# Optimization experiments

Hardware: AMD Instinct MI355X
Metric: run time of the kernel (lower is better)

## Reference

```python
import jax, jax.numpy as jnp
import numpy as np

CE_W, DICE_W, BD_W = 1.0, 3.0, 2.0   # combined-loss lambdas
BPW = 10.0                            # boundary pixel weight
SMOOTH = 1e-6                         # dice smoothing
# cv2.getStructuringElement(cv2.MORPH_ELLIPSE, (5,5))
ELLIPSE5 = np.array([[0,0,1,0,0],
                     [1,1,1,1,1],
                     [1,1,1,1,1],
                     [1,1,1,1,1],
                     [0,0,1,0,0]], dtype=bool)


def setup_inputs() -> dict:
    key = jax.random.key(0)
    k1, k2 = jax.random.split(key)
    B, C, H, W = 8, 8, 512, 1024
    pred = jax.random.normal(k1, (B, C, H, W), dtype=jnp.float32)
    target = jax.random.randint(k2, (B, H, W), 0, C).astype(jnp.int32)
    return {"pred": pred, "target": target}


def _morph(mask, is_dilate):
    """Grayscale dilate/erode with 5x5 ellipse SE (matches cv2 default border:
    padding value never wins the max/min)."""
    pad_val = 0 if is_dilate else jnp.iinfo(jnp.int32).max
    p = jnp.pad(mask, ((0, 0), (2, 2), (2, 2)), constant_values=pad_val)
    H, W = mask.shape[1], mask.shape[2]
    out = None
    for dy in range(5):
        for dx in range(5):
            if not ELLIPSE5[dy, dx]:
                continue
            s = p[:, dy:dy + H, dx:dx + W]
            if out is None:
                out = s
            else:
                out = jnp.maximum(out, s) if is_dilate else jnp.minimum(out, s)
    return out


def reference(pred, target):
    B, C, H, W = pred.shape
    logp = jax.nn.log_softmax(pred, axis=1)                         # (B,C,H,W)
    # per-pixel cross entropy
    ce_map = -jnp.take_along_axis(logp, target[:, None], axis=1)[:, 0]  # (B,H,W)
    ce = ce_map.mean()
    # dice over softmax probs vs one-hot target
    probs = jnp.exp(logp)
    onehot = jax.nn.one_hot(target, C, dtype=pred.dtype, axis=1)    # (B,C,H,W)
    inter = jnp.sum(probs * onehot, axis=(2, 3))                    # (B,C)
    card = jnp.sum(probs, axis=(2, 3)) + jnp.sum(onehot, axis=(2, 3))
    dice = 1.0 - jnp.mean((2.0 * inter + SMOOTH) / (card + SMOOTH))
    # boundary mask = morphological gradient of the label map
    t = target.astype(jnp.int32)
    boundary = _morph(t, True) - _morph(t, False)                   # (B,H,W)
    wmap = jnp.where(boundary > 0, jnp.float32(BPW), jnp.float32(1.0))
    bd = jnp.mean(ce_map * wmap)
    return CE_W * ce + DICE_W * dice + BD_W * bd
```

## Files before the change

### kernel.cpp

```cpp
#include <hip/hip_runtime.h>
#include <math.h>

constexpr int B = 8, C = 8, H = 512, W = 1024;
constexpr int RH = 2;
constexpr int NT = 256;
constexpr float BPW = 10.0f;
constexpr float SMOOTH = 1e-6f;

constexpr int ACC_N = 2 + 3 * B * C;

__device__ __forceinline__ unsigned win_or5(unsigned lo, unsigned mid, unsigned hi) {
    unsigned long long a = ((unsigned long long)mid << 32) | lo;
    unsigned long long b = ((unsigned long long)hi << 32) | mid;
    return (unsigned)(a >> 16) | (unsigned)(a >> 24) | mid |
           (unsigned)(b >> 8) | (unsigned)(b >> 16);
}

__device__ __forceinline__ unsigned pack_row(const int* __restrict__ tb, int gh, int gc) {
    if (gh < 0 || gh >= H || gc < 0 || gc >= W) return 0u;
    const int4 t4 = *reinterpret_cast<const int4*>(tb + (size_t)gh * W + gc);
    return (1u << t4.x) | ((1u << t4.y) << 8) | ((1u << t4.z) << 16) | ((1u << t4.w) << 24);
}

__global__ __launch_bounds__(NT)
void loss_main(const float* __restrict__ pred, const int* __restrict__ target,
               float* __restrict__ acc) {
    __shared__ float sred[4][26];

    const int tid = threadIdx.x;
    const int h0 = blockIdx.x * RH;
    const int b  = blockIdx.y;
    const int gc = tid * 4;

    const int* tb = target + (size_t)b * H * W;
    const size_t plane = (size_t)H * W;
    const float* pb = pred + (size_t)b * C * plane + (size_t)h0 * W + gc;

    const unsigned c0 = pack_row(tb, h0 - 2, gc);
    const unsigned c1 = pack_row(tb, h0 - 1, gc);
    const unsigned c2 = pack_row(tb, h0,     gc);
    const unsigned c3 = pack_row(tb, h0 + 1, gc);
    const unsigned c4 = pack_row(tb, h0 + 2, gc);
    const unsigned c5 = pack_row(tb, h0 + 3, gc);
    const unsigned l0 = pack_row(tb, h0 - 1, gc - 4);
    const unsigned l1 = pack_row(tb, h0,     gc - 4);
    const unsigned l2 = pack_row(tb, h0 + 1, gc - 4);
    const unsigned l3 = pack_row(tb, h0 + 2, gc - 4);
    const unsigned r0 = pack_row(tb, h0 - 1, gc + 4);
    const unsigned r1 = pack_row(tb, h0,     gc + 4);
    const unsigned r2 = pack_row(tb, h0 + 1, gc + 4);
    const unsigned r3 = pack_row(tb, h0 + 2, gc + 4);

    float4 xa[C], xb[C];
#pragma unroll
    for (int c = 0; c < C; ++c) xa[c] = *reinterpret_cast<const float4*>(pb + c * plane);
#pragma unroll
    for (int c = 0; c < C; ++c) xb[c] = *reinterpret_cast<const float4*>(pb + c * plane + W);

    float ce_s = 0.f, bd_s = 0.f;
    float p_s[C], in_s[C];
    unsigned cnt = 0u;
#pragma unroll
    for (int c = 0; c < C; ++c) { p_s[c] = 0.f; in_s[c] = 0.f; }

    const unsigned bmA = win_or5(l0 | l1 | l2, c1 | c2 | c3, r0 | r1 | r2) | c0 | c4;
    const unsigned bmB = win_or5(l1 | l2 | l3, c2 | c3 | c4, r1 | r2 | r3) | c1 | c5;

#pragma unroll
    for (int s = 0; s < 2; ++s) {
        const float4* x = (s == 0) ? xa : xb;
        const unsigned cmid = (s == 0) ? c2 : c3;
        const unsigned bm4  = (s == 0) ? bmA : bmB;

#pragma unroll
        for (int j = 0; j < 4; ++j) {
            const float x0 = (j==0)?x[0].x:(j==1)?x[0].y:(j==2)?x[0].z:x[0].w;
            const float x1 = (j==0)?x[1].x:(j==1)?x[1].y:(j==2)?x[1].z:x[1].w;
            const float x2 = (j==0)?x[2].x:(j==1)?x[2].y:(j==2)?x[2].z:x[2].w;
            const float x3 = (j==0)?x[3].x:(j==1)?x[3].y:(j==2)?x[3].z:x[3].w;
            const float x4 = (j==0)?x[4].x:(j==1)?x[4].y:(j==2)?x[4].z:x[4].w;
            const float x5 = (j==0)?x[5].x:(j==1)?x[5].y:(j==2)?x[5].z:x[5].w;
            const float x6 = (j==0)?x[6].x:(j==1)?x[6].y:(j==2)?x[6].z:x[6].w;
            const float x7 = (j==0)?x[7].x:(j==1)?x[7].y:(j==2)?x[7].z:x[7].w;

            const float e0 = __expf(x0), e1 = __expf(x1), e2 = __expf(x2), e3 = __expf(x3);
            const float e4 = __expf(x4), e5 = __expf(x5), e6 = __expf(x6), e7 = __expf(x7);
            const float sum = ((e0 + e1) + (e2 + e3)) + ((e4 + e5) + (e6 + e7));
            const float invs = __builtin_amdgcn_rcpf(sum);

            const unsigned cm  = (cmid >> (8 * j)) & 0xFFu;
            const unsigned bmj = (bm4  >> (8 * j)) & 0xFFu;
            const int t = 31 - __clz(cm);

            const float p0 = e0 * invs, p1 = e1 * invs, p2 = e2 * invs, p3 = e3 * invs;
            const float p4 = e4 * invs, p5 = e5 * invs, p6 = e6 * invs, p7 = e7 * invs;
            p_s[0] += p0; p_s[1] += p1; p_s[2] += p2; p_s[3] += p3;
            p_s[4] += p4; p_s[5] += p5; p_s[6] += p6; p_s[7] += p7;

            const bool b0 = (t == 0), b1 = (t == 1), b2 = (t == 2), b3 = (t == 3);
            const bool b4 = (t == 4), b5 = (t == 5), b6 = (t == 6), b7 = (t == 7);
            in_s[0] += b0 ? p0 : 0.f;  in_s[1] += b1 ? p1 : 0.f;
            in_s[2] += b2 ? p2 : 0.f;  in_s[3] += b3 ? p3 : 0.f;
            in_s[4] += b4 ? p4 : 0.f;  in_s[5] += b5 ? p5 : 0.f;
            in_s[6] += b6 ? p6 : 0.f;  in_s[7] += b7 ? p7 : 0.f;

            float pt = p0;
            pt = b1 ? p1 : pt;  pt = b2 ? p2 : pt;  pt = b3 ? p3 : pt;
            pt = b4 ? p4 : pt;  pt = b5 ? p5 : pt;  pt = b6 ? p6 : pt;
            pt = b7 ? p7 : pt;
            const float l = __logf(pt);
            const float wgt = (bmj & (bmj - 1u)) ? BPW : 1.f;
            ce_s -= l;
            bd_s = fmaf(-l, wgt, bd_s);
            cnt += 1u << (t << 2);
        }
    }

    float vals[26];
    vals[0] = ce_s; vals[1] = bd_s;
#pragma unroll
    for (int c = 0; c < C; ++c) {
        vals[2 + c]  = p_s[c];
        vals[10 + c] = in_s[c];
        vals[18 + c] = (float)((cnt >> (4 * c)) & 0xFu);
    }
#pragma unroll
    for (int k = 0; k < 26; ++k) {
        float v = vals[k];
#pragma unroll
        for (int off = 32; off > 0; off >>= 1) v += __shfl_down(v, off, 64);
        vals[k] = v;
    }
    const int lane = tid & 63, wid = tid >> 6;
    if (lane == 0) {
#pragma unroll
        for (int k = 0; k < 26; ++k) sred[wid][k] = vals[k];
    }
    __syncthreads();
    if (tid < 26) {
        const float v = sred[0][tid] + sred[1][tid] + sred[2][tid] + sred[3][tid];
        int gi;
        if (tid == 0)       gi = 0;
        else if (tid == 1)  gi = 1;
        else if (tid < 10)  gi = 2 + b * C + (tid - 2);
        else if (tid < 18)  gi = 2 + B * C + b * C + (tid - 10);
        else                gi = 2 + 2 * B * C + b * C + (tid - 18);
        atomicAdd(&acc[gi], v);
    }
}

__global__ void loss_final(const float* __restrict__ acc, float* __restrict__ out) {
    const int i = threadIdx.x;
    const float psum  = acc[2 + i];
    const float inter = acc[2 + B * C + i];
    const float cnt   = acc[2 + 2 * B * C + i];
    float d = (2.f * inter + SMOOTH) / (psum + cnt + SMOOTH);
#pragma unroll
    for (int off = 32; off > 0; off >>= 1) d += __shfl_down(d, off, 64);
    if (i == 0) {
        const float N = (float)B * H * W;
        const float ce = acc[0] / N;
        const float bd = acc[1] / N;
        const float dice = 1.f - d / (float)(B * C);
        out[0] = 1.0f * ce + 3.0f * dice + 2.0f * bd;
    }
}

extern "C" void kernel_launch(void* const* d_in, const int* in_sizes, int n_in,
                              void* d_out, int out_size, void* d_ws, size_t ws_size,
                              hipStream_t stream) {
    const float* pred = (const float*)d_in[0];
    const int* target = (const int*)d_in[1];
    float* acc = (float*)d_ws;
    float* out = (float*)d_out;

    hipMemsetAsync(acc, 0, ACC_N * sizeof(float), stream);

    dim3 grid(H / RH, B);
    loss_main<<<grid, NT, 0, stream>>>(pred, target, acc);
    loss_final<<<1, 64, 0, stream>>>(acc, out);
}
```

Before: 211.5 us.

## Stage packed label halo in LDS, process four rows per block, swizzle blocks

Each block now handles four rows instead of two. It packs the eight-row label halo into shared memory as one-hot bytes, so the left and right neighbour windows are read from LDS rather than through redundant global loads. Block indices are swizzled so that neighbouring launches fall in different images, and launch bounds request four blocks per SM. The cross-lane reduction is reshaped to finish with partial shuffles plus a strided LDS pass, which cuts the number of shuffle steps. The costs are an extra __syncthreads, more LDS use, and fewer blocks in flight.

```diff
diff --git a/kernel.cpp b/kernel.cpp
--- a/kernel.cpp
+++ b/kernel.cpp
@@ -2,12 +2,17 @@
 #include <math.h>
 
 constexpr int B = 8, C = 8, H = 512, W = 1024;
-constexpr int RH = 2;
+constexpr int RH = 4;
 constexpr int NT = 256;
 constexpr float BPW = 10.0f;
 constexpr float SMOOTH = 1e-6f;
 
 constexpr int ACC_N = 2 + 3 * B * C;
+
+constexpr int TROWS = RH + 4;
+constexpr int TSTRIDE = W + 8;
+constexpr int NVALS = 26;
+constexpr int PSTRIDE = 28;
 
 __device__ __forceinline__ unsigned win_or5(unsigned lo, unsigned mid, unsigned hi) {
     unsigned long long a = ((unsigned long long)mid << 32) | lo;
@@ -16,61 +21,68 @@
            (unsigned)(b >> 8) | (unsigned)(b >> 16);
 }
 
-__device__ __forceinline__ unsigned pack_row(const int* __restrict__ tb, int gh, int gc) {
-    if (gh < 0 || gh >= H || gc < 0 || gc >= W) return 0u;
-    const int4 t4 = *reinterpret_cast<const int4*>(tb + (size_t)gh * W + gc);
-    return (1u << t4.x) | ((1u << t4.y) << 8) | ((1u << t4.z) << 16) | ((1u << t4.w) << 24);
-}
-
-__global__ __launch_bounds__(NT)
+__global__ __launch_bounds__(NT, 4)
 void loss_main(const float* __restrict__ pred, const int* __restrict__ target,
                float* __restrict__ acc) {
-    __shared__ float sred[4][26];
+    __shared__ unsigned char tgt[TROWS * TSTRIDE];
+    __shared__ float sred[32 * PSTRIDE];
 
     const int tid = threadIdx.x;
-    const int h0 = blockIdx.x * RH;
-    const int b  = blockIdx.y;
+    const int lin = blockIdx.x + blockIdx.y * gridDim.x;
+    const int swz = (lin & 7) * 128 + (lin >> 3);
+    const int h0 = (swz & 127) * RH;
+    const int b  = swz >> 7;
     const int gc = tid * 4;
 
     const int* tb = target + (size_t)b * H * W;
     const size_t plane = (size_t)H * W;
-    const float* pb = pred + (size_t)b * C * plane + (size_t)h0 * W + gc;
-
-    const unsigned c0 = pack_row(tb, h0 - 2, gc);
-    const unsigned c1 = pack_row(tb, h0 - 1, gc);
-    const unsigned c2 = pack_row(tb, h0,     gc);
-    const unsigned c3 = pack_row(tb, h0 + 1, gc);
-    const unsigned c4 = pack_row(tb, h0 + 2, gc);
-    const unsigned c5 = pack_row(tb, h0 + 3, gc);
-    const unsigned l0 = pack_row(tb, h0 - 1, gc - 4);
-    const unsigned l1 = pack_row(tb, h0,     gc - 4);
-    const unsigned l2 = pack_row(tb, h0 + 1, gc - 4);
-    const unsigned l3 = pack_row(tb, h0 + 2, gc - 4);
-    const unsigned r0 = pack_row(tb, h0 - 1, gc + 4);
-    const unsigned r1 = pack_row(tb, h0,     gc + 4);
-    const unsigned r2 = pack_row(tb, h0 + 1, gc + 4);
-    const unsigned r3 = pack_row(tb, h0 + 2, gc + 4);
-
-    float4 xa[C], xb[C];
-#pragma unroll
-    for (int c = 0; c < C; ++c) xa[c] = *reinterpret_cast<const float4*>(pb + c * plane);
-#pragma unroll
-    for (int c = 0; c < C; ++c) xb[c] = *reinterpret_cast<const float4*>(pb + c * plane + W);
+
+    if (tid < 2 * TROWS) {
+        const int r = tid >> 1;
+        *reinterpret_cast<unsigned*>(&tgt[r * TSTRIDE + ((tid & 1) ? (4 + W) : 0)]) = 0u;
+    }
+#pragma unroll
+    for (int r = 0; r < TROWS; ++r) {
+        const int gh = h0 - 2 + r;
+        unsigned m = 0u;
+        if (gh >= 0 && gh < H) {
+            const int4 t4 = *reinterpret_cast<const int4*>(tb + (size_t)gh * W + gc);
+            m = (1u << t4.x) | ((1u << t4.y) << 8) | ((1u << t4.z) << 16) | ((1u << t4.w) << 24);
+        }
+        *reinterpret_cast<unsigned*>(&tgt[r * TSTRIDE + 4 + gc]) = m;
+    }
+    __syncthreads();
+
+    unsigned M[TROWS], L[TROWS], R[TROWS];
+#pragma unroll
+    for (int r = 0; r < TROWS; ++r)
+        M[r] = *reinterpret_cast<const unsigned*>(&tgt[r * TSTRIDE + 4 + gc]);
+#pragma unroll
+    for (int r = 1; r < TROWS - 1; ++r) {
+        L[r] = *reinterpret_cast<const unsigned*>(&tgt[r * TSTRIDE + gc]);
+        R[r] = *reinterpret_cast<const unsigned*>(&tgt[r * TSTRIDE + 8 + gc]);
+    }
 
     float ce_s = 0.f, bd_s = 0.f;
     float p_s[C], in_s[C];
-    unsigned cnt = 0u;
+    unsigned long long cnt = 0ull;
 #pragma unroll
     for (int c = 0; c < C; ++c) { p_s[c] = 0.f; in_s[c] = 0.f; }
 
-    const unsigned bmA = win_or5(l0 | l1 | l2, c1 | c2 | c3, r0 | r1 | r2) | c0 | c4;
-    const unsigned bmB = win_or5(l1 | l2 | l3, c2 | c3 | c4, r1 | r2 | r3) | c1 | c5;
-
-#pragma unroll
-    for (int s = 0; s < 2; ++s) {
-        const float4* x = (s == 0) ? xa : xb;
-        const unsigned cmid = (s == 0) ? c2 : c3;
-        const unsigned bm4  = (s == 0) ? bmA : bmB;
+    const float* pbase = pred + (size_t)b * C * plane + (size_t)h0 * W + gc;
+
+#pragma unroll
+    for (int s = 0; s < RH; ++s) {
+        float4 x[C];
+#pragma unroll
+        for (int c = 0; c < C; ++c)
+            x[c] = *reinterpret_cast<const float4*>(pbase + (size_t)c * plane + (size_t)s * W);
+
+        const unsigned Lor = L[s + 1] | L[s + 2] | L[s + 3];
+        const unsigned Mor = M[s + 1] | M[s + 2] | M[s + 3];
+        const unsigned Ror = R[s + 1] | R[s + 2] | R[s + 3];
+        const unsigned bm4  = win_or5(Lor, Mor, Ror) | M[s] | M[s + 4];
+        const unsigned cmid = M[s + 2];
 
 #pragma unroll
         for (int j = 0; j < 4; ++j) {
@@ -112,40 +124,50 @@
             const float wgt = (bmj & (bmj - 1u)) ? BPW : 1.f;
             ce_s -= l;
             bd_s = fmaf(-l, wgt, bd_s);
-            cnt += 1u << (t << 2);
+            cnt += 1ull << (t << 3);
         }
     }
 
-    float vals[26];
+    float vals[NVALS];
     vals[0] = ce_s; vals[1] = bd_s;
 #pragma unroll
     for (int c = 0; c < C; ++c) {
         vals[2 + c]  = p_s[c];
         vals[10 + c] = in_s[c];
-        vals[18 + c] = (float)((cnt >> (4 * c)) & 0xFu);
-    }
-#pragma unroll
-    for (int k = 0; k < 26; ++k) {
+        vals[18 + c] = (float)((unsigned)((cnt >> (8 * c)) & 0xFFull));
+    }
+#pragma unroll
+    for (int k = 0; k < NVALS; ++k) {
         float v = vals[k];
-#pragma unroll
-        for (int off = 32; off > 0; off >>= 1) v += __shfl_down(v, off, 64);
+        v += __shfl_down(v, 32, 64);
+        v += __shfl_down(v, 16, 64);
+        v += __shfl_down(v, 8, 64);
         vals[k] = v;
     }
     const int lane = tid & 63, wid = tid >> 6;
-    if (lane == 0) {
-#pragma unroll
-        for (int k = 0; k < 26; ++k) sred[wid][k] = vals[k];
+    if (lane < 8) {
+        const int p = wid * 8 + lane;
+#pragma unroll
+        for (int k = 0; k < NVALS; ++k) sred[p * PSTRIDE + k] = vals[k];
     }
     __syncthreads();
-    if (tid < 26) {
-        const float v = sred[0][tid] + sred[1][tid] + sred[2][tid] + sred[3][tid];
-        int gi;
-        if (tid == 0)       gi = 0;
-        else if (tid == 1)  gi = 1;
-        else if (tid < 10)  gi = 2 + b * C + (tid - 2);
-        else if (tid < 18)  gi = 2 + B * C + b * C + (tid - 10);
-        else                gi = 2 + 2 * B * C + b * C + (tid - 18);
-        atomicAdd(&acc[gi], v);
+
+    const int k = tid >> 3, j = tid & 7;
+    if (k < NVALS) {
+        float v = sred[(0 * 8 + j) * PSTRIDE + k] + sred[(1 * 8 + j) * PSTRIDE + k]
+                + sred[(2 * 8 + j) * PSTRIDE + k] + sred[(3 * 8 + j) * PSTRIDE + k];
+        v += __shfl_down(v, 4, 64);
+        v += __shfl_down(v, 2, 64);
+        v += __shfl_down(v, 1, 64);
+        if (j == 0) {
+            int gi;
+            if (k == 0)       gi = 0;
+            else if (k == 1)  gi = 1;
+            else if (k < 10)  gi = 2 + b * C + (k - 2);
+            else if (k < 18)  gi = 2 + B * C + b * C + (k - 10);
+            else              gi = 2 + 2 * B * C + b * C + (k - 18);
+            atomicAdd(&acc[gi], v);
+        }
     }
 }
 
```

Result: slower. 253.5 us (+19.8%).

## Swizzle block order, issue pred loads first, and shorten the block reduction

Applied to the files above, without the earlier changes.

Remaps the linear block index so consecutive blocks cover different batches, spreading traffic and atomic targets. The pred loads are now issued before the target packing so their latency overlaps. The cross-lane reduction is cut to three shuffle steps with eight partials per wave, finished by a second shuffle stage across 176 threads. Pairs of class counts are packed into one float to reduce the number of reduced values. This trims reduction overhead, which is small next to the memory-bound main loop, and relies on float packing staying exact for counts up to 4096.

```diff
diff --git a/kernel.cpp b/kernel.cpp
--- a/kernel.cpp
+++ b/kernel.cpp
@@ -9,6 +9,9 @@
 
 constexpr int ACC_N = 2 + 3 * B * C;
 
+constexpr int NVALS = 22;
+constexpr int PSTRIDE = 24;
+
 __device__ __forceinline__ unsigned win_or5(unsigned lo, unsigned mid, unsigned hi) {
     unsigned long long a = ((unsigned long long)mid << 32) | lo;
     unsigned long long b = ((unsigned long long)hi << 32) | mid;
@@ -25,16 +28,24 @@
 __global__ __launch_bounds__(NT)
 void loss_main(const float* __restrict__ pred, const int* __restrict__ target,
                float* __restrict__ acc) {
-    __shared__ float sred[4][26];
+    __shared__ float sred[32 * PSTRIDE];
 
     const int tid = threadIdx.x;
-    const int h0 = blockIdx.x * RH;
-    const int b  = blockIdx.y;
+    const int lin = blockIdx.x + blockIdx.y * gridDim.x;
+    const int swz = (lin & 7) * 256 + (lin >> 3);
+    const int h0 = (swz & 255) * RH;
+    const int b  = swz >> 8;
     const int gc = tid * 4;
 
     const int* tb = target + (size_t)b * H * W;
     const size_t plane = (size_t)H * W;
     const float* pb = pred + (size_t)b * C * plane + (size_t)h0 * W + gc;
+
+    float4 xa[C], xb[C];
+#pragma unroll
+    for (int c = 0; c < C; ++c) xa[c] = *reinterpret_cast<const float4*>(pb + c * plane);
+#pragma unroll
+    for (int c = 0; c < C; ++c) xb[c] = *reinterpret_cast<const float4*>(pb + c * plane + W);
 
     const unsigned c0 = pack_row(tb, h0 - 2, gc);
     const unsigned c1 = pack_row(tb, h0 - 1, gc);
@@ -51,12 +62,6 @@
     const unsigned r2 = pack_row(tb, h0 + 1, gc + 4);
     const unsigned r3 = pack_row(tb, h0 + 2, gc + 4);
 
-    float4 xa[C], xb[C];
-#pragma unroll
-    for (int c = 0; c < C; ++c) xa[c] = *reinterpret_cast<const float4*>(pb + c * plane);
-#pragma unroll
-    for (int c = 0; c < C; ++c) xb[c] = *reinterpret_cast<const float4*>(pb + c * plane + W);
-
     float ce_s = 0.f, bd_s = 0.f;
     float p_s[C], in_s[C];
     unsigned cnt = 0u;
@@ -116,36 +121,55 @@
         }
     }
 
-    float vals[26];
+    float vals[NVALS];
     vals[0] = ce_s; vals[1] = bd_s;
 #pragma unroll
     for (int c = 0; c < C; ++c) {
         vals[2 + c]  = p_s[c];
         vals[10 + c] = in_s[c];
-        vals[18 + c] = (float)((cnt >> (4 * c)) & 0xFu);
-    }
-#pragma unroll
-    for (int k = 0; k < 26; ++k) {
+    }
+#pragma unroll
+    for (int q = 0; q < 4; ++q) {
+        const float lo = (float)((cnt >> (8 * q)) & 0xFu);
+        const float hi = (float)((cnt >> (8 * q + 4)) & 0xFu);
+        vals[18 + q] = lo + 4096.f * hi;
+    }
+#pragma unroll
+    for (int k = 0; k < NVALS; ++k) {
         float v = vals[k];
-#pragma unroll
-        for (int off = 32; off > 0; off >>= 1) v += __shfl_down(v, off, 64);
+        v += __shfl_down(v, 32, 64);
+        v += __shfl_down(v, 16, 64);
+        v += __shfl_down(v, 8, 64);
         vals[k] = v;
     }
     const int lane = tid & 63, wid = tid >> 6;
-    if (lane == 0) {
-#pragma unroll
-        for (int k = 0; k < 26; ++k) sred[wid][k] = vals[k];
+    if (lane < 8) {
+        const int p = wid * 8 + lane;
+#pragma unroll
+        for (int k = 0; k < NVALS; ++k) sred[p * PSTRIDE + k] = vals[k];
     }
     __syncthreads();
-    if (tid < 26) {
-        const float v = sred[0][tid] + sred[1][tid] + sred[2][tid] + sred[3][tid];
-        int gi;
-        if (tid == 0)       gi = 0;
-        else if (tid == 1)  gi = 1;
-        else if (tid < 10)  gi = 2 + b * C + (tid - 2);
-        else if (tid < 18)  gi = 2 + B * C + b * C + (tid - 10);
-        else                gi = 2 + 2 * B * C + b * C + (tid - 18);
-        atomicAdd(&acc[gi], v);
+
+    const int k = tid >> 3, j = tid & 7;
+    if (k < NVALS) {
+        float v = sred[(0 * 8 + j) * PSTRIDE + k] + sred[(1 * 8 + j) * PSTRIDE + k]
+                + sred[(2 * 8 + j) * PSTRIDE + k] + sred[(3 * 8 + j) * PSTRIDE + k];
+        v += __shfl_down(v, 4, 64);
+        v += __shfl_down(v, 2, 64);
+        v += __shfl_down(v, 1, 64);
+        if (j == 0) {
+            if (k == 0)      atomicAdd(&acc[0], v);
+            else if (k == 1) atomicAdd(&acc[1], v);
+            else if (k < 10) atomicAdd(&acc[2 + b * C + (k - 2)], v);
+            else if (k < 18) atomicAdd(&acc[2 + B * C + b * C + (k - 10)], v);
+            else {
+                const int q = k - 18;
+                const float hi = floorf(v * (1.f / 4096.f));
+                const float lo = v - 4096.f * hi;
+                atomicAdd(&acc[2 + 2 * B * C + b * C + 2 * q],     lo);
+                atomicAdd(&acc[2 + 2 * B * C + b * C + 2 * q + 1], hi);
+            }
+        }
     }
 }
 
```

Measured after the change: 248.1 us. 17.3% more time.
